# Kernel optimization log

Hardware: AMD Instinct MI355X
Metric: run time of the kernel (lower is better)

The kernel has to match this reference:

```python
import jax, jax.numpy as jnp
import numpy as np

N_HEADS = 16

def setup_inputs() -> dict:
    key = jax.random.key(0)
    ks = jax.random.split(key, 7)
    B, S, D = 2, 2048, 1024
    sc = 0.02
    return {
        "x": jax.random.normal(ks[0], (B, S, D), dtype=jnp.float32),
        "Wq": jax.random.normal(ks[1], (D, D), dtype=jnp.float32) * sc,
        "bq": jax.random.normal(ks[2], (D,), dtype=jnp.float32) * sc,
        "Wk": jax.random.normal(ks[3], (D, D), dtype=jnp.float32) * sc,
        "bk": jax.random.normal(ks[4], (D,), dtype=jnp.float32) * sc,
        "Wv": jax.random.normal(ks[5], (D, D), dtype=jnp.float32) * sc,
        "bv": jax.random.normal(ks[6], (D,), dtype=jnp.float32) * sc,
    }

def reference(x, Wq, bq, Wk, bk, Wv, bv):
    B, S, D = x.shape
    H = N_HEADS
    W = D // H  # head width
    # torch Linear: y = x @ W.T + b
    q = x @ Wq.T + bq
    k = x @ Wk.T + bk
    v = x @ Wv.T + bv
    # split last dim into (H, W) and move heads forward: (B, H, S, W)
    q = q.reshape(B, S, H, W).transpose(0, 2, 1, 3)
    k = k.reshape(B, S, H, W).transpose(0, 2, 1, 3)
    v = v.reshape(B, S, H, W).transpose(0, 2, 1, 3)
    scores = jnp.einsum("bhqw,bhkw->bhqk", q, k) / jnp.sqrt(jnp.asarray(W, x.dtype))
    # original applies softmax, (dropout=identity at eval), then softmax AGAIN
    scores = jax.nn.softmax(scores, axis=-1)
    scores = jax.nn.softmax(scores, axis=-1)
    h = jnp.einsum("bhqk,bhkw->bhqw", scores, v)
    h = h.transpose(0, 2, 1, 3).reshape(B, S, D)
    return h
```

## Files before the change

kernel.cpp:

```cpp
#include <hip/hip_runtime.h>
#include <cstdint>
#include <cstddef>

typedef __bf16 bf16_t;
typedef __bf16 bf16x2 __attribute__((ext_vector_type(2)));
typedef __bf16 bf16x4 __attribute__((ext_vector_type(4)));
typedef __bf16 bf16x8 __attribute__((ext_vector_type(8)));
typedef float f32x4 __attribute__((ext_vector_type(4)));
typedef unsigned int u32x2 __attribute__((ext_vector_type(2)));

typedef __attribute__((address_space(1))) unsigned int gu32;
typedef __attribute__((address_space(3))) unsigned int lu32;

#define MFMA16(a, b, c) __builtin_amdgcn_mfma_f32_16x16x32_bf16((a), (b), (c), 0, 0, 0)

__device__ __forceinline__ void gload_lds16(const void* g, void* l) {
    __builtin_amdgcn_global_load_lds((gu32*)const_cast<void*>(g), (lu32*)l, 16, 0, 0);
}

__global__ __launch_bounds__(256) void cvt_bf16(
    const float* __restrict__ x, const float* __restrict__ Wq,
    const float* __restrict__ Wk, const float* __restrict__ Wv,
    bf16_t* __restrict__ xb, bf16_t* __restrict__ Wqb,
    bf16_t* __restrict__ Wkb, bf16_t* __restrict__ Wvb)
{
    const int z = blockIdx.z;
    const float* src = (z == 0) ? x : (z == 1) ? Wq : (z == 2) ? Wk : Wv;
    bf16_t* dst      = (z == 0) ? xb : (z == 1) ? Wqb : (z == 2) ? Wkb : Wvb;
    const int n = (z == 0) ? 4096 * 1024 : 1024 * 1024;
    const int stride = gridDim.x * blockDim.x * 4;
    for (int i = (blockIdx.x * blockDim.x + threadIdx.x) * 4; i < n; i += stride) {
        const float4 f = *(const float4*)(src + i);
        bf16x4 o; o[0] = (bf16_t)f.x; o[1] = (bf16_t)f.y; o[2] = (bf16_t)f.z; o[3] = (bf16_t)f.w;
        *(bf16x4*)(dst + i) = o;
    }
}

__global__ __launch_bounds__(512) void qkv_gemm_bf16(
    const bf16_t* __restrict__ xb,
    const bf16_t* __restrict__ W0b, const float* __restrict__ b0,
    const bf16_t* __restrict__ W1b, const float* __restrict__ b1,
    const bf16_t* __restrict__ W2b, const float* __restrict__ b2,
    bf16_t* __restrict__ Qo, bf16_t* __restrict__ Ko, bf16_t* __restrict__ VTo,
    float* __restrict__ Vp)
{
    const int z = blockIdx.z;
    const bf16_t* Wm = (z == 0) ? W0b : (z == 1) ? W1b : W2b;
    const float* bia = (z == 0) ? b0 : (z == 1) ? b1 : b2;

    __shared__ bf16_t As[2][128 * 32];
    __shared__ bf16_t Bs[2][128 * 32];

    const int tid  = threadIdx.x;
    const int lane = tid & 63;
    const int wv   = tid >> 6;
    const int quad = lane >> 4;
    const int l16  = lane & 15;
    const int wm   = wv >> 1;
    const int wn   = wv & 1;
    const int m0   = blockIdx.x * 128;
    const int n0   = blockIdx.y * 128;

    const int rs = tid >> 2;
    const int gs = ((tid & 3) ^ ((rs >> 1) & 3)) * 8;
    const int fp = (quad ^ ((l16 >> 1) & 3)) * 8;

    f32x4 acc[2][4];
    for (int i = 0; i < 2; i++)
        for (int j = 0; j < 4; j++) acc[i][j] = (f32x4)0.0f;

    gload_lds16(xb + (size_t)(m0 + rs) * 1024 + gs, &As[0][(wv * 64) * 8]);
    gload_lds16(Wm + (size_t)(n0 + rs) * 1024 + gs, &Bs[0][(wv * 64) * 8]);

#pragma unroll 2
    for (int kt = 0; kt < 32; kt++) {
        const int cur = kt & 1, nxt = cur ^ 1;
        __syncthreads();
        if (kt < 31) {
            const int kp = (kt + 1) * 32;
            gload_lds16(xb + (size_t)(m0 + rs) * 1024 + kp + gs, &As[nxt][(wv * 64) * 8]);
            gload_lds16(Wm + (size_t)(n0 + rs) * 1024 + kp + gs, &Bs[nxt][(wv * 64) * 8]);
        }
        bf16x8 af[2], bfr[4];
        for (int mt = 0; mt < 2; mt++)
            af[mt] = *(const bf16x8*)&As[cur][(wm * 32 + mt * 16 + l16) * 32 + fp];
        for (int nt = 0; nt < 4; nt++)
            bfr[nt] = *(const bf16x8*)&Bs[cur][(wn * 64 + nt * 16 + l16) * 32 + fp];
        for (int mt = 0; mt < 2; mt++)
            for (int nt = 0; nt < 4; nt++)
                acc[mt][nt] = MFMA16(af[mt], bfr[nt], acc[mt][nt]);
    }

    float bv[4];
    for (int nt = 0; nt < 4; nt++)
        bv[nt] = bia[n0 + wn * 64 + nt * 16 + l16];

    if (z < 2) {
        bf16_t* out = (z == 0) ? Qo : Ko;
        const float scl = (z == 0) ? 0.125f : 1.0f;
        for (int mt = 0; mt < 2; mt++) {
            const int mrow = m0 + wm * 32 + mt * 16 + quad * 4;
            for (int nt = 0; nt < 4; nt++) {
                const int n = n0 + wn * 64 + nt * 16 + l16;
                for (int r = 0; r < 4; r++)
                    out[(size_t)(mrow + r) * 1024 + n] = (bf16_t)((acc[mt][nt][r] + bv[nt]) * scl);
            }
        }
    } else {
        const int h = blockIdx.y * 2 + wn;
        float psum[4] = {0.f, 0.f, 0.f, 0.f};
        for (int mt = 0; mt < 2; mt++) {
            const int sg = m0 + wm * 32 + mt * 16 + quad * 4;
            const int bb = sg >> 11;
            const int s  = sg & 2047;
            for (int nt = 0; nt < 4; nt++) {
                const int w = nt * 16 + l16;
                bf16x4 pk;
                for (int r = 0; r < 4; r++) {
                    pk[r] = (bf16_t)(acc[mt][nt][r] + bv[nt]);
                    psum[nt] += (float)pk[r];
                }
                *(bf16x4*)(VTo + ((size_t)((bb * 16 + h) * 64 + w)) * 2048 + s) = pk;
            }
        }
        for (int nt = 0; nt < 4; nt++) {
            psum[nt] += __shfl_xor(psum[nt], 16, 64);
            psum[nt] += __shfl_xor(psum[nt], 32, 64);
        }
        float* red = (float*)&As[0][0];
        if (quad == 0)
            for (int nt = 0; nt < 4; nt++)
                red[(wv * 4 + nt) * 16 + l16] = psum[nt];
        __syncthreads();
        if (wm == 0 && quad == 0) {
            const int bb = m0 >> 11;
            const int j  = blockIdx.x & 15;
            for (int nt = 0; nt < 4; nt++) {
                float s4 = ((red[((wn + 0) * 4 + nt) * 16 + l16]
                           + red[((wn + 2) * 4 + nt) * 16 + l16])
                           + red[((wn + 4) * 4 + nt) * 16 + l16])
                           + red[((wn + 6) * 4 + nt) * 16 + l16];
                Vp[((size_t)((bb * 16 + h) * 64 + nt * 16 + l16)) * 16 + j] = s4;
            }
        }
    }
}

__global__ __launch_bounds__(512, 4) void attn(
    const bf16_t* __restrict__ Qg, const bf16_t* __restrict__ Kg,
    const bf16_t* __restrict__ VTg, const float* __restrict__ Vp,
    float* __restrict__ out)
{
    const int qt = blockIdx.x;
    const int h  = blockIdx.y;
    const int b  = blockIdx.z;

    const int tid  = threadIdx.x;
    const int wv   = tid >> 6;
    const int lane = tid & 63;
    const int quad = lane >> 4;
    const int l16  = lane & 15;
    const int qg   = wv >> 1;
    const int sh   = wv & 1;

    const size_t base  = ((size_t)b * 2048) * 1024 + (size_t)h * 64;
    const size_t vbase = ((size_t)(b * 16 + h) * 64) * 2048;
    const int q0 = qt * 128;

    __shared__ __align__(16) unsigned char smem[49152];
    bf16_t* Qs = (bf16_t*)smem;

    {
        const int c0 = tid, c1 = 512 + tid;
        const int r0 = c0 >> 3, g0 = ((c0 & 7) ^ (r0 & 7)) * 8;
        const int r1 = c1 >> 3, g1 = ((c1 & 7) ^ (r1 & 7)) * 8;
        gload_lds16(Qg + base + (size_t)(q0 + r0) * 1024 + g0, Qs + (wv * 64) * 8);
        gload_lds16(Qg + base + (size_t)(q0 + r1) * 1024 + g1, Qs + (512 + wv * 64) * 8);
    }
    const int rk = tid >> 3;
    const int gk = ((tid & 7) ^ (rk & 7)) * 8;
    gload_lds16(Kg + base + (size_t)rk * 1024 + gk,
                (bf16_t*)(smem + 16384) + (wv * 64) * 8);
    gload_lds16(VTg + vbase + (size_t)rk * 2048 + gk,
                (bf16_t*)(smem + 32768) + (wv * 64) * 8);

    const int fs0 = ((0 ^ quad) ^ (l16 & 7)) * 8;
    const int fs1 = ((4 ^ quad) ^ (l16 & 7)) * 8;
    const int fsA = sh ? fs1 : fs0;

    const int qr0 = qg * 32 + l16;
    const int qr1 = qg * 32 + 16 + l16;

    f32x4 oa[2][4], l1acc[2];
    for (int qs = 0; qs < 2; qs++) {
        for (int nt = 0; nt < 4; nt++) oa[qs][nt] = (f32x4)0.0f;
        l1acc[qs] = (f32x4)0.0f;
    }

    bf16x8 ones;
    for (int j = 0; j < 8; j++) ones[j] = (bf16_t)1.0f;

    __syncthreads();

    bf16x8 aq[2][2];
    aq[0][0] = *(const bf16x8*)&Qs[qr0 * 64 + fs0];
    aq[0][1] = *(const bf16x8*)&Qs[qr0 * 64 + fs1];
    aq[1][0] = *(const bf16x8*)&Qs[qr1 * 64 + fs0];
    aq[1][1] = *(const bf16x8*)&Qs[qr1 * 64 + fs1];

    bf16x8 af[2];
    bf16x8 bvf[4];

    #define EXCHANGE_P(PS_SA)                                                   \
        for (int qs = 0; qs < 2; qs++) {                                        \
            union { bf16x2 h; unsigned int u; } t00, t01, t10, t11;             \
            t00.h[0] = (bf16_t)__expf(PS_SA[0][qs][0]);                         \
            t00.h[1] = (bf16_t)__expf(PS_SA[0][qs][1]);                         \
            t01.h[0] = (bf16_t)__expf(PS_SA[0][qs][2]);                         \
            t01.h[1] = (bf16_t)__expf(PS_SA[0][qs][3]);                         \
            t10.h[0] = (bf16_t)__expf(PS_SA[1][qs][0]);                         \
            t10.h[1] = (bf16_t)__expf(PS_SA[1][qs][1]);                         \
            t11.h[0] = (bf16_t)__expf(PS_SA[1][qs][2]);                         \
            t11.h[1] = (bf16_t)__expf(PS_SA[1][qs][3]);                         \
            u32x2 p0 = __builtin_amdgcn_permlane32_swap(t00.u, t10.u, false, false); \
            u32x2 q0p = __builtin_amdgcn_permlane16_swap(p0[0], p0[1], false, false); \
            u32x2 p1 = __builtin_amdgcn_permlane32_swap(t01.u, t11.u, false, false); \
            u32x2 q1p = __builtin_amdgcn_permlane16_swap(p1[0], p1[1], false, false); \
            union { unsigned int u[4]; bf16x8 h; } w;                           \
            w.u[0] = q0p[0]; w.u[1] = q1p[0]; w.u[2] = q0p[1]; w.u[3] = q1p[1]; \
            af[qs] = w.h;                                                       \
        }

    {
        const bf16_t* Ks0 = (const bf16_t*)(smem + 16384);
        const bf16_t* Vs0 = (const bf16_t*)(smem + 32768);
        gload_lds16(Kg + base + (size_t)(64 + rk) * 1024 + gk,
                    (bf16_t*)(smem + 24576) + (wv * 64) * 8);
        gload_lds16(VTg + vbase + (size_t)rk * 2048 + 64 + gk,
                    (bf16_t*)(smem + 40960) + (wv * 64) * 8);

        f32x4 sa[2][2];
        for (int st = 0; st < 2; st++)
            for (int qs = 0; qs < 2; qs++) sa[st][qs] = (f32x4)0.0f;
        for (int st = 0; st < 2; st++) {
            const int srow = (sh * 32 + st * 16 + l16) * 64;
            bf16x8 kb0 = *(const bf16x8*)&Ks0[srow + fs0];
            bf16x8 kb1 = *(const bf16x8*)&Ks0[srow + fs1];
            for (int qs = 0; qs < 2; qs++) {
                sa[st][qs] = MFMA16(kb0, aq[qs][0], sa[st][qs]);
                sa[st][qs] = MFMA16(kb1, aq[qs][1], sa[st][qs]);
            }
        }
        EXCHANGE_P(sa)
        for (int nt = 0; nt < 4; nt++)
            bvf[nt] = *(const bf16x8*)&Vs0[(nt * 16 + l16) * 64 + fsA];
    }

#pragma unroll 2
    for (int kt = 1; kt < 32; kt++) {
        const int cur = kt & 1, prv = cur ^ 1;
        const bf16_t* KsC = (const bf16_t*)(smem + 16384 + cur * 8192);
        const bf16_t* VsC = (const bf16_t*)(smem + 32768 + cur * 8192);
        __syncthreads();

        if (kt < 31) {
            gload_lds16(Kg + base + (size_t)((kt + 1) * 64 + rk) * 1024 + gk,
                        (bf16_t*)(smem + 16384 + prv * 8192) + (wv * 64) * 8);
            gload_lds16(VTg + vbase + (size_t)rk * 2048 + (kt + 1) * 64 + gk,
                        (bf16_t*)(smem + 32768 + prv * 8192) + (wv * 64) * 8);
        }

        f32x4 sa[2][2];
        for (int st = 0; st < 2; st++)
            for (int qs = 0; qs < 2; qs++) sa[st][qs] = (f32x4)0.0f;
        for (int st = 0; st < 2; st++) {
            const int srow = (sh * 32 + st * 16 + l16) * 64;
            bf16x8 kb0 = *(const bf16x8*)&KsC[srow + fs0];
            bf16x8 kb1 = *(const bf16x8*)&KsC[srow + fs1];
            for (int qs = 0; qs < 2; qs++) {
                sa[st][qs] = MFMA16(kb0, aq[qs][0], sa[st][qs]);
                sa[st][qs] = MFMA16(kb1, aq[qs][1], sa[st][qs]);
            }
        }

        l1acc[0] = MFMA16(af[0], ones, l1acc[0]);
        l1acc[1] = MFMA16(af[1], ones, l1acc[1]);
        for (int nt = 0; nt < 4; nt++) {
            oa[0][nt] = MFMA16(af[0], bvf[nt], oa[0][nt]);
            oa[1][nt] = MFMA16(af[1], bvf[nt], oa[1][nt]);
        }

        for (int nt = 0; nt < 4; nt++)
            bvf[nt] = *(const bf16x8*)&VsC[(nt * 16 + l16) * 64 + fsA];

        EXCHANGE_P(sa)
    }

    {
        l1acc[0] = MFMA16(af[0], ones, l1acc[0]);
        l1acc[1] = MFMA16(af[1], ones, l1acc[1]);
        for (int nt = 0; nt < 4; nt++) {
            oa[0][nt] = MFMA16(af[0], bvf[nt], oa[0][nt]);
            oa[1][nt] = MFMA16(af[1], bvf[nt], oa[1][nt]);
        }
    }

    __syncthreads();
    f32x4* R4 = (f32x4*)smem;
    f32x4* L4 = (f32x4*)(smem + 32768);
    const int bi = qg * 64 + lane;
    if (sh == 1) {
        for (int qs = 0; qs < 2; qs++)
            for (int nt = 0; nt < 4; nt++)
                R4[bi * 8 + ((qs * 4 + nt) ^ (lane & 7))] = oa[qs][nt];
        L4[bi * 2 + 0] = l1acc[0];
        L4[bi * 2 + 1] = l1acc[1];
    }
    __syncthreads();
    if (sh == 0) {
        for (int qs = 0; qs < 2; qs++)
            for (int nt = 0; nt < 4; nt++)
                oa[qs][nt] += R4[bi * 8 + ((qs * 4 + nt) ^ (lane & 7))];
        l1acc[0] += L4[bi * 2 + 0];
        l1acc[1] += L4[bi * 2 + 1];

        float invq[2][4];
        for (int qs = 0; qs < 2; qs++)
            for (int r = 0; r < 4; r++) invq[qs][r] = 1.0f / l1acc[qs][r];

        float vs[4];
        const size_t vprow = (size_t)(b * 16 + h) * 64;
        for (int nt = 0; nt < 4; nt++) {
            const f32x4 p4 = *(const f32x4*)&Vp[(vprow + nt * 16 + l16) * 16 + quad * 4];
            float t = (p4[0] + p4[1]) + (p4[2] + p4[3]);
            t += __shfl_xor(t, 16, 64);
            t += __shfl_xor(t, 32, 64);
            vs[nt] = t;
        }

        const float inv_denom = 1.0f / 2049.0f;
        for (int qs = 0; qs < 2; qs++)
            for (int nt = 0; nt < 4; nt++)
                for (int r = 0; r < 4; r++) {
                    const int srow = q0 + qg * 32 + qs * 16 + quad * 4 + r;
                    out[((size_t)b * 2048 + srow) * 1024 + (size_t)h * 64 + nt * 16 + l16] =
                        (vs[nt] + oa[qs][nt][r] * invq[qs][r]) * inv_denom;
                }
    }
    #undef EXCHANGE_P
}

extern "C" void kernel_launch(void* const* d_in, const int* in_sizes, int n_in,
                              void* d_out, int out_size, void* d_ws, size_t ws_size,
                              hipStream_t stream) {
    const float* x  = (const float*)d_in[0];
    const float* Wq = (const float*)d_in[1];
    const float* bq = (const float*)d_in[2];
    const float* Wk = (const float*)d_in[3];
    const float* bk = (const float*)d_in[4];
    const float* Wv = (const float*)d_in[5];
    const float* bv = (const float*)d_in[6];

    bf16_t* Qw  = (bf16_t*)d_ws;
    bf16_t* Kw  = Qw + (size_t)4096 * 1024;
    bf16_t* VTw = Kw + (size_t)4096 * 1024;
    float*  Vp  = (float*)(VTw + (size_t)4096 * 1024);

    bf16_t* xb  = (bf16_t*)d_out;
    bf16_t* Wqb = xb + (size_t)4096 * 1024;
    bf16_t* Wkb = Wqb + (size_t)1024 * 1024;
    bf16_t* Wvb = Wkb + (size_t)1024 * 1024;

    cvt_bf16<<<dim3(1024, 1, 4), 256, 0, stream>>>(x, Wq, Wk, Wv, xb, Wqb, Wkb, Wvb);
    qkv_gemm_bf16<<<dim3(32, 8, 3), 512, 0, stream>>>(
        xb, Wqb, bq, Wkb, bk, Wvb, bv, Qw, Kw, VTw, Vp);
    attn<<<dim3(16, 16, 2), 512, 0, stream>>>(Qw, Kw, VTw, Vp, (float*)d_out);
}
```

Before: 163.9 us.

## Double attention query tile to 256 rows and use exp2 with folded log2e scale

The attention kernel now processes 256 query rows per block instead of 128, so each wave handles four 16-row query slices and every K/V tile loaded into LDS is reused across twice as many queries. LDS grows to 64KB, launch bounds drop to 2 blocks per SM, and the grid halves to 512 blocks. Separately, log2(e) is folded into the Q scale so the softmax uses exp2f instead of __expf. The cost is higher register pressure and fewer, larger blocks, which may hurt occupancy and load balance, plus extra syncs in the final reduction.

```diff
diff --git a/kernel.cpp b/kernel.cpp
--- a/kernel.cpp
+++ b/kernel.cpp
@@ -97,7 +97,7 @@
 
     if (z < 2) {
         bf16_t* out = (z == 0) ? Qo : Ko;
-        const float scl = (z == 0) ? 0.125f : 1.0f;
+        const float scl = (z == 0) ? 0.18033688011112042f : 1.0f;
         for (int mt = 0; mt < 2; mt++) {
             const int mrow = m0 + wm * 32 + mt * 16 + quad * 4;
             for (int nt = 0; nt < 4; nt++) {
@@ -146,7 +146,7 @@
     }
 }
 
-__global__ __launch_bounds__(512, 4) void attn(
+__global__ __launch_bounds__(512, 2) void attn(
     const bf16_t* __restrict__ Qg, const bf16_t* __restrict__ Kg,
     const bf16_t* __restrict__ VTg, const float* __restrict__ Vp,
     float* __restrict__ out)
@@ -165,34 +165,30 @@
 
     const size_t base  = ((size_t)b * 2048) * 1024 + (size_t)h * 64;
     const size_t vbase = ((size_t)(b * 16 + h) * 64) * 2048;
-    const int q0 = qt * 128;
-
-    __shared__ __align__(16) unsigned char smem[49152];
+    const int q0 = qt * 256;
+
+    __shared__ __align__(16) unsigned char smem[65536];
     bf16_t* Qs = (bf16_t*)smem;
 
-    {
-        const int c0 = tid, c1 = 512 + tid;
-        const int r0 = c0 >> 3, g0 = ((c0 & 7) ^ (r0 & 7)) * 8;
-        const int r1 = c1 >> 3, g1 = ((c1 & 7) ^ (r1 & 7)) * 8;
-        gload_lds16(Qg + base + (size_t)(q0 + r0) * 1024 + g0, Qs + (wv * 64) * 8);
-        gload_lds16(Qg + base + (size_t)(q0 + r1) * 1024 + g1, Qs + (512 + wv * 64) * 8);
+    for (int i = 0; i < 4; i++) {
+        const int c = i * 512 + tid;
+        const int r = c >> 3, g = ((c & 7) ^ (r & 7)) * 8;
+        gload_lds16(Qg + base + (size_t)(q0 + r) * 1024 + g,
+                    Qs + (i * 512 + wv * 64) * 8);
     }
     const int rk = tid >> 3;
     const int gk = ((tid & 7) ^ (rk & 7)) * 8;
     gload_lds16(Kg + base + (size_t)rk * 1024 + gk,
-                (bf16_t*)(smem + 16384) + (wv * 64) * 8);
+                (bf16_t*)(smem + 32768) + (wv * 64) * 8);
     gload_lds16(VTg + vbase + (size_t)rk * 2048 + gk,
-                (bf16_t*)(smem + 32768) + (wv * 64) * 8);
+                (bf16_t*)(smem + 49152) + (wv * 64) * 8);
 
     const int fs0 = ((0 ^ quad) ^ (l16 & 7)) * 8;
     const int fs1 = ((4 ^ quad) ^ (l16 & 7)) * 8;
     const int fsA = sh ? fs1 : fs0;
 
-    const int qr0 = qg * 32 + l16;
-    const int qr1 = qg * 32 + 16 + l16;
-
-    f32x4 oa[2][4], l1acc[2];
-    for (int qs = 0; qs < 2; qs++) {
+    f32x4 oa[4][4], l1acc[4];
+    for (int qs = 0; qs < 4; qs++) {
         for (int nt = 0; nt < 4; nt++) oa[qs][nt] = (f32x4)0.0f;
         l1acc[qs] = (f32x4)0.0f;
     }
@@ -202,51 +198,52 @@
 
     __syncthreads();
 
-    bf16x8 aq[2][2];
-    aq[0][0] = *(const bf16x8*)&Qs[qr0 * 64 + fs0];
-    aq[0][1] = *(const bf16x8*)&Qs[qr0 * 64 + fs1];
-    aq[1][0] = *(const bf16x8*)&Qs[qr1 * 64 + fs0];
-    aq[1][1] = *(const bf16x8*)&Qs[qr1 * 64 + fs1];
-
-    bf16x8 af[2];
+    bf16x8 aq[4][2];
+    for (int qs = 0; qs < 4; qs++) {
+        const int qr = (qg * 64 + qs * 16 + l16) * 64;
+        aq[qs][0] = *(const bf16x8*)&Qs[qr + fs0];
+        aq[qs][1] = *(const bf16x8*)&Qs[qr + fs1];
+    }
+
+    bf16x8 af[4];
     bf16x8 bvf[4];
 
     #define EXCHANGE_P(PS_SA)                                                   \
-        for (int qs = 0; qs < 2; qs++) {                                        \
+        for (int qs = 0; qs < 4; qs++) {                                        \
             union { bf16x2 h; unsigned int u; } t00, t01, t10, t11;             \
-            t00.h[0] = (bf16_t)__expf(PS_SA[0][qs][0]);                         \
-            t00.h[1] = (bf16_t)__expf(PS_SA[0][qs][1]);                         \
-            t01.h[0] = (bf16_t)__expf(PS_SA[0][qs][2]);                         \
-            t01.h[1] = (bf16_t)__expf(PS_SA[0][qs][3]);                         \
-            t10.h[0] = (bf16_t)__expf(PS_SA[1][qs][0]);                         \
-            t10.h[1] = (bf16_t)__expf(PS_SA[1][qs][1]);                         \
-            t11.h[0] = (bf16_t)__expf(PS_SA[1][qs][2]);                         \
-            t11.h[1] = (bf16_t)__expf(PS_SA[1][qs][3]);                         \
+            t00.h[0] = (bf16_t)exp2f(PS_SA[0][qs][0]);                          \
+            t00.h[1] = (bf16_t)exp2f(PS_SA[0][qs][1]);                          \
+            t01.h[0] = (bf16_t)exp2f(PS_SA[0][qs][2]);                          \
+            t01.h[1] = (bf16_t)exp2f(PS_SA[0][qs][3]);                          \
+            t10.h[0] = (bf16_t)exp2f(PS_SA[1][qs][0]);                          \
+            t10.h[1] = (bf16_t)exp2f(PS_SA[1][qs][1]);                          \
+            t11.h[0] = (bf16_t)exp2f(PS_SA[1][qs][2]);                          \
+            t11.h[1] = (bf16_t)exp2f(PS_SA[1][qs][3]);                          \
             u32x2 p0 = __builtin_amdgcn_permlane32_swap(t00.u, t10.u, false, false); \
-            u32x2 q0p = __builtin_amdgcn_permlane16_swap(p0[0], p0[1], false, false); \
+            u32x2 e0 = __builtin_amdgcn_permlane16_swap(p0[0], p0[1], false, false); \
             u32x2 p1 = __builtin_amdgcn_permlane32_swap(t01.u, t11.u, false, false); \
-            u32x2 q1p = __builtin_amdgcn_permlane16_swap(p1[0], p1[1], false, false); \
+            u32x2 e1 = __builtin_amdgcn_permlane16_swap(p1[0], p1[1], false, false); \
             union { unsigned int u[4]; bf16x8 h; } w;                           \
-            w.u[0] = q0p[0]; w.u[1] = q1p[0]; w.u[2] = q0p[1]; w.u[3] = q1p[1]; \
+            w.u[0] = e0[0]; w.u[1] = e1[0]; w.u[2] = e0[1]; w.u[3] = e1[1];     \
             af[qs] = w.h;                                                       \
         }
 
     {
-        const bf16_t* Ks0 = (const bf16_t*)(smem + 16384);
-        const bf16_t* Vs0 = (const bf16_t*)(smem + 32768);
+        const bf16_t* Ks0 = (const bf16_t*)(smem + 32768);
+        const bf16_t* Vs0 = (const bf16_t*)(smem + 49152);
         gload_lds16(Kg + base + (size_t)(64 + rk) * 1024 + gk,
-                    (bf16_t*)(smem + 24576) + (wv * 64) * 8);
+                    (bf16_t*)(smem + 40960) + (wv * 64) * 8);
         gload_lds16(VTg + vbase + (size_t)rk * 2048 + 64 + gk,
-                    (bf16_t*)(smem + 40960) + (wv * 64) * 8);
-
-        f32x4 sa[2][2];
+                    (bf16_t*)(smem + 57344) + (wv * 64) * 8);
+
+        f32x4 sa[2][4];
         for (int st = 0; st < 2; st++)
-            for (int qs = 0; qs < 2; qs++) sa[st][qs] = (f32x4)0.0f;
+            for (int qs = 0; qs < 4; qs++) sa[st][qs] = (f32x4)0.0f;
         for (int st = 0; st < 2; st++) {
             const int srow = (sh * 32 + st * 16 + l16) * 64;
             bf16x8 kb0 = *(const bf16x8*)&Ks0[srow + fs0];
             bf16x8 kb1 = *(const bf16x8*)&Ks0[srow + fs1];
-            for (int qs = 0; qs < 2; qs++) {
+            for (int qs = 0; qs < 4; qs++) {
                 sa[st][qs] = MFMA16(kb0, aq[qs][0], sa[st][qs]);
                 sa[st][qs] = MFMA16(kb1, aq[qs][1], sa[st][qs]);
             }
@@ -259,36 +256,35 @@
 #pragma unroll 2
     for (int kt = 1; kt < 32; kt++) {
         const int cur = kt & 1, prv = cur ^ 1;
-        const bf16_t* KsC = (const bf16_t*)(smem + 16384 + cur * 8192);
-        const bf16_t* VsC = (const bf16_t*)(smem + 32768 + cur * 8192);
+        const bf16_t* KsC = (const bf16_t*)(smem + 32768 + cur * 8192);
+        const bf16_t* VsC = (const bf16_t*)(smem + 49152 + cur * 8192);
         __syncthreads();
 
         if (kt < 31) {
             gload_lds16(Kg + base + (size_t)((kt + 1) * 64 + rk) * 1024 + gk,
-                        (bf16_t*)(smem + 16384 + prv * 8192) + (wv * 64) * 8);
+                        (bf16_t*)(smem + 32768 + prv * 8192) + (wv * 64) * 8);
             gload_lds16(VTg + vbase + (size_t)rk * 2048 + (kt + 1) * 64 + gk,
-                        (bf16_t*)(smem + 32768 + prv * 8192) + (wv * 64) * 8);
-        }
-
-        f32x4 sa[2][2];
+                        (bf16_t*)(smem + 49152 + prv * 8192) + (wv * 64) * 8);
+        }
+
+        f32x4 sa[2][4];
         for (int st = 0; st < 2; st++)
-            for (int qs = 0; qs < 2; qs++) sa[st][qs] = (f32x4)0.0f;
+            for (int qs = 0; qs < 4; qs++) sa[st][qs] = (f32x4)0.0f;
         for (int st = 0; st < 2; st++) {
             const int srow = (sh * 32 + st * 16 + l16) * 64;
             bf16x8 kb0 = *(const bf16x8*)&KsC[srow + fs0];
             bf16x8 kb1 = *(const bf16x8*)&KsC[srow + fs1];
-            for (int qs = 0; qs < 2; qs++) {
+            for (int qs = 0; qs < 4; qs++) {
                 sa[st][qs] = MFMA16(kb0, aq[qs][0], sa[st][qs]);
                 sa[st][qs] = MFMA16(kb1, aq[qs][1], sa[st][qs]);
             }
         }
 
-        l1acc[0] = MFMA16(af[0], ones, l1acc[0]);
-        l1acc[1] = MFMA16(af[1], ones, l1acc[1]);
-        for (int nt = 0; nt < 4; nt++) {
-            oa[0][nt] = MFMA16(af[0], bvf[nt], oa[0][nt]);
-            oa[1][nt] = MFMA16(af[1], bvf[nt], oa[1][nt]);
-        }
+        for (int qs = 0; qs < 4; qs++)
+            l1acc[qs] = MFMA16(af[qs], ones, l1acc[qs]);
+        for (int nt = 0; nt < 4; nt++)
+            for (int qs = 0; qs < 4; qs++)
+                oa[qs][nt] = MFMA16(af[qs], bvf[nt], oa[qs][nt]);
 
         for (int nt = 0; nt < 4; nt++)
             bvf[nt] = *(const bf16x8*)&VsC[(nt * 16 + l16) * 64 + fsA];
@@ -297,35 +293,39 @@
     }
 
     {
-        l1acc[0] = MFMA16(af[0], ones, l1acc[0]);
-        l1acc[1] = MFMA16(af[1], ones, l1acc[1]);
-        for (int nt = 0; nt < 4; nt++) {
-            oa[0][nt] = MFMA16(af[0], bvf[nt], oa[0][nt]);
-            oa[1][nt] = MFMA16(af[1], bvf[nt], oa[1][nt]);
-        }
+        for (int qs = 0; qs < 4; qs++)
+            l1acc[qs] = MFMA16(af[qs], ones, l1acc[qs]);
+        for (int nt = 0; nt < 4; nt++)
+            for (int qs = 0; qs < 4; qs++)
+                oa[qs][nt] = MFMA16(af[qs], bvf[nt], oa[qs][nt]);
     }
 
     __syncthreads();
     f32x4* R4 = (f32x4*)smem;
-    f32x4* L4 = (f32x4*)(smem + 32768);
     const int bi = qg * 64 + lane;
     if (sh == 1) {
-        for (int qs = 0; qs < 2; qs++)
-            for (int nt = 0; nt < 4; nt++)
-                R4[bi * 8 + ((qs * 4 + nt) ^ (lane & 7))] = oa[qs][nt];
-        L4[bi * 2 + 0] = l1acc[0];
-        L4[bi * 2 + 1] = l1acc[1];
+        for (int qs = 0; qs < 4; qs++)
+            for (int nt = 0; nt < 4; nt++)
+                R4[bi * 16 + ((qs * 4 + nt) ^ (lane & 15))] = oa[qs][nt];
     }
     __syncthreads();
     if (sh == 0) {
-        for (int qs = 0; qs < 2; qs++)
-            for (int nt = 0; nt < 4; nt++)
-                oa[qs][nt] += R4[bi * 8 + ((qs * 4 + nt) ^ (lane & 7))];
-        l1acc[0] += L4[bi * 2 + 0];
-        l1acc[1] += L4[bi * 2 + 1];
-
-        float invq[2][4];
-        for (int qs = 0; qs < 2; qs++)
+        for (int qs = 0; qs < 4; qs++)
+            for (int nt = 0; nt < 4; nt++)
+                oa[qs][nt] += R4[bi * 16 + ((qs * 4 + nt) ^ (lane & 15))];
+    }
+    __syncthreads();
+    if (sh == 1) {
+        for (int qs = 0; qs < 4; qs++)
+            R4[bi * 4 + (qs ^ (lane & 3))] = l1acc[qs];
+    }
+    __syncthreads();
+    if (sh == 0) {
+        for (int qs = 0; qs < 4; qs++)
+            l1acc[qs] += R4[bi * 4 + (qs ^ (lane & 3))];
+
+        float invq[4][4];
+        for (int qs = 0; qs < 4; qs++)
             for (int r = 0; r < 4; r++) invq[qs][r] = 1.0f / l1acc[qs][r];
 
         float vs[4];
@@ -339,10 +339,10 @@
         }
 
         const float inv_denom = 1.0f / 2049.0f;
-        for (int qs = 0; qs < 2; qs++)
+        for (int qs = 0; qs < 4; qs++)
             for (int nt = 0; nt < 4; nt++)
                 for (int r = 0; r < 4; r++) {
-                    const int srow = q0 + qg * 32 + qs * 16 + quad * 4 + r;
+                    const int srow = q0 + qg * 64 + qs * 16 + quad * 4 + r;
                     out[((size_t)b * 2048 + srow) * 1024 + (size_t)h * 64 + nt * 16 + l16] =
                         (vs[nt] + oa[qs][nt][r] * invq[qs][r]) * inv_denom;
                 }
@@ -374,5 +374,5 @@
     cvt_bf16<<<dim3(1024, 1, 4), 256, 0, stream>>>(x, Wq, Wk, Wv, xb, Wqb, Wkb, Wvb);
     qkv_gemm_bf16<<<dim3(32, 8, 3), 512, 0, stream>>>(
         xb, Wqb, bq, Wkb, bk, Wvb, bv, Qw, Kw, VTw, Vp);
-    attn<<<dim3(16, 16, 2), 512, 0, stream>>>(Qw, Kw, VTw, Vp, (float*)d_out);
-}
+    attn<<<dim3(8, 16, 2), 512, 0, stream>>>(Qw, Kw, VTw, Vp, (float*)d_out);
+}
```

After: 170.6 us. 1.04x slower.
